# Kernel tuning notes

Measured on AMD Instinct MI355X. Metric: run time of the kernel, lower is better.

## Reference

```python
import jax, jax.numpy as jnp
import numpy as np

N, F, U, R, B, M = 8192, 64, 64, 4, 20, 512


def setup_inputs() -> dict:
    key = jax.random.key(0)
    ks = jax.random.split(key, 6)
    features = jax.random.normal(ks[0], (1, N, F), dtype=jnp.float32)
    out_indices = jax.random.randint(ks[1], (1, M), 0, N, dtype=jnp.int64)
    # normalized adjacency per relation; scale keeps activations O(1)
    adjacency = jax.random.uniform(ks[2], (R, N, N), dtype=jnp.float32) / N
    bases = jax.random.normal(ks[3], (F, U, B), dtype=jnp.float32) * (1.0 / np.sqrt(F * B))
    coefficients = jax.random.normal(ks[4], (R, B), dtype=jnp.float32)
    self_kernel = jax.random.normal(ks[5], (F, U), dtype=jnp.float32) * (1.0 / np.sqrt(F))
    bias = jnp.zeros((U,), dtype=jnp.float32)
    return {
        "features": features,
        "out_indices": out_indices,
        "adjacency": adjacency,
        "bases": bases,
        "coefficients": coefficients,
        "self_kernel": self_kernel,
        "bias": bias,
    }


def reference(features, out_indices, adjacency, bases, coefficients, self_kernel, bias):
    # features: (1, N, F); adjacency: (R, N, N)
    x = features[0]  # (N, F) -- full-batch, batch dim is 1
    # basis decomposition: W_r = sum_k bases[:, :, k] * coeff[r, k]
    W = jnp.einsum("fuk,rk->rfu", bases, coefficients)  # (R, F, U)
    xw = jnp.einsum("nf,rfu->rnu", x, W)               # (R, N, U)
    agg = jnp.einsum("rnm,rmu->nu", adjacency, xw)      # sum_r A_r @ (X W_r)
    out = agg + x @ self_kernel + bias                   # (N, U)
    out = jax.nn.relu(out)
    # final_layer=False: return all node features with batch dim restored
    return out[None]  # (1, N, U)
```

## Files before the change

### kernel.cpp

```cpp
#include <hip/hip_runtime.h>


typedef float v4f __attribute__((ext_vector_type(4)));
typedef unsigned int v4u __attribute__((ext_vector_type(4)));
typedef short v8s __attribute__((ext_vector_type(8)));

__device__ __forceinline__ unsigned short f2bf(float f) {
  unsigned int u = __builtin_bit_cast(unsigned int, f);
  return (unsigned short)((u + 0x7fffu + ((u >> 16) & 1u)) >> 16);
}

__device__ __forceinline__ void gload16(const void* g, void* l) {
  __builtin_amdgcn_global_load_lds((const __attribute__((address_space(1))) void*)g,
                                   (__attribute__((address_space(3))) void*)l, 16, 0, 0);
}

__device__ __forceinline__ void gload16nt(const void* g, void* l) {
  __builtin_amdgcn_global_load_lds((const __attribute__((address_space(1))) void*)g,
                                   (__attribute__((address_space(3))) void*)l, 16, 0, 2);
}

__global__ __launch_bounds__(256) void rgcn_wk(const float* __restrict__ bases,
                                               const float* __restrict__ coef,
                                               float* __restrict__ W) {
  int i = blockIdx.x * 256 + threadIdx.x;
  int r = i >> 12;
  int fu = i & 4095;
  float s = 0.f;
#pragma unroll
  for (int k = 0; k < 20; ++k) s += bases[fu * 20 + k] * coef[r * 20 + k];
  W[i] = s;
}

__global__ __launch_bounds__(256) void rgcn_prep(const float* __restrict__ x,
                                                 const float* __restrict__ W,
                                                 const float* __restrict__ sk,
                                                 const float* __restrict__ bias,
                                                 unsigned short* __restrict__ xwf,
                                                 float* __restrict__ selfout) {
  __shared__ float lx[2048];
  __shared__ unsigned short lxw[8192];
  const int t = threadIdx.x;
  const int blk = blockIdx.x;
  const int n0 = blk * 32;
  for (int i = t; i < 2048; i += 256) lx[i] = x[(size_t)n0 * 64 + i];
  __syncthreads();
  const int u = t & 63, rq = t >> 6;
  float acc[8][5];
#pragma unroll
  for (int p = 0; p < 8; ++p)
#pragma unroll
    for (int c = 0; c < 5; ++c) acc[p][c] = 0.f;
  const float* wu = W + u;
  const float* sku = sk + u;
#pragma unroll 4
  for (int f = 0; f < 64; ++f) {
    float w0 = wu[f * 64];
    float w1 = wu[4096 + f * 64];
    float w2 = wu[8192 + f * 64];
    float w3 = wu[12288 + f * 64];
    float w4 = sku[f * 64];
#pragma unroll
    for (int p = 0; p < 8; ++p) {
      float xv = lx[(rq * 8 + p) * 64 + f];
      acc[p][0] += xv * w0;
      acc[p][1] += xv * w1;
      acc[p][2] += xv * w2;
      acc[p][3] += xv * w3;
      acc[p][4] += xv * w4;
    }
  }
  const float bu = bias[u];
#pragma unroll
  for (int p = 0; p < 8; ++p) {
    int km = rq * 8 + p;
    selfout[(size_t)(n0 + km) * 64 + u] = acc[p][4] + bu;
    int idx = (u >> 4) * 512 + ((km >> 3) * 16 + (u & 15)) * 8 + (km & 7);
#pragma unroll
    for (int r = 0; r < 4; ++r) lxw[r * 2048 + idx] = f2bf(acc[p][r]);
  }
  __syncthreads();
  const unsigned int* lsrc = (const unsigned int*)lxw;
  unsigned int* gdst = (unsigned int*)xwf;
  for (int i = t; i < 4096; i += 256) {
    int r = i >> 10, q = i & 1023;
    gdst[(size_t)(r * 256 + blk) * 1024 + q] = lsrc[i];
  }
}


#define PACK8(S, X0, X1)          \
  {                               \
    S[0] = (short)f2bf(X0.x);     \
    S[1] = (short)f2bf(X0.y);     \
    S[2] = (short)f2bf(X0.z);     \
    S[3] = (short)f2bf(X0.w);     \
    S[4] = (short)f2bf(X1.x);     \
    S[5] = (short)f2bf(X1.y);     \
    S[6] = (short)f2bf(X1.z);     \
    S[7] = (short)f2bf(X1.w);     \
  }

#define STAGE(P)                                          \
  {                                                       \
    char* ab = Wb + (P)*16384;                            \
    gload16nt(aps0, ab);                                  \
    gload16nt(aps1, ab + 1024);                           \
    gload16nt(aps2, ab + 2048);                           \
    gload16nt(aps3, ab + 3072);                           \
    gload16nt(aps4, ab + 4096);                           \
    gload16nt(aps5, ab + 5120);                           \
    gload16nt(aps6, ab + 6144);                           \
    gload16nt(aps7, ab + 7168);                           \
    char* bb = ab + 8192;                                 \
    gload16(bsrc, bb);                                    \
    gload16(bsrc + 512, bb + 1024);                       \
    gload16(bsrc + 1024, bb + 2048);                      \
    gload16(bsrc + 1536, bb + 3072);                      \
    gload16(bsrc + 2048, bb + 4096);                      \
    gload16(bsrc + 2560, bb + 5120);                      \
    gload16(bsrc + 3072, bb + 6144);                      \
    gload16(bsrc + 3584, bb + 7168);                      \
    aps0 += 64; aps1 += 64; aps2 += 64; aps3 += 64;       \
    aps4 += 64; aps5 += 64; aps6 += 64; aps7 += 64;       \
    bsrc += 4096;                                         \
  }

#define MFMA8(AF0, AF1, B0, B1, B2, B3)                                          \
  {                                                                              \
    acc00 = __builtin_amdgcn_mfma_f32_16x16x32_bf16(AF0, B0, acc00, 0, 0, 0);    \
    acc01 = __builtin_amdgcn_mfma_f32_16x16x32_bf16(AF0, B1, acc01, 0, 0, 0);    \
    acc02 = __builtin_amdgcn_mfma_f32_16x16x32_bf16(AF0, B2, acc02, 0, 0, 0);    \
    acc03 = __builtin_amdgcn_mfma_f32_16x16x32_bf16(AF0, B3, acc03, 0, 0, 0);    \
    acc10 = __builtin_amdgcn_mfma_f32_16x16x32_bf16(AF1, B0, acc10, 0, 0, 0);    \
    acc11 = __builtin_amdgcn_mfma_f32_16x16x32_bf16(AF1, B1, acc11, 0, 0, 0);    \
    acc12 = __builtin_amdgcn_mfma_f32_16x16x32_bf16(AF1, B2, acc12, 0, 0, 0);    \
    acc13 = __builtin_amdgcn_mfma_f32_16x16x32_bf16(AF1, B3, acc13, 0, 0, 0);    \
  }

#define STEP(P, VMN, DO_STAGE)                                             \
  {                                                                        \
    asm volatile("s_waitcnt vmcnt(" #VMN ")" ::: "memory");                \
    __builtin_amdgcn_sched_barrier(0);                                     \
    const char* ap = Wb + (P)*16384;                                       \
    const char* bp = ap + 8192;                                            \
    v4f a000 = *(const v4f*)(ap + ao000);                                  \
    v4f a001 = *(const v4f*)(ap + ao001);                                  \
    v4f a010 = *(const v4f*)(ap + ao010);                                  \
    v4f a011 = *(const v4f*)(ap + ao011);                                  \
    v4f a100 = *(const v4f*)(ap + ao100);                                  \
    v4f a101 = *(const v4f*)(ap + ao101);                                  \
    v4f a110 = *(const v4f*)(ap + ao110);                                  \
    v4f a111 = *(const v4f*)(ap + ao111);                                  \
    v4u b00 = *(const v4u*)(bp + bo);                                      \
    v4u b01 = *(const v4u*)(bp + bo + 1024);                               \
    v4u b02 = *(const v4u*)(bp + bo + 2048);                               \
    v4u b03 = *(const v4u*)(bp + bo + 3072);                               \
    v4u b10 = *(const v4u*)(bp + bo + 4096);                               \
    v4u b11 = *(const v4u*)(bp + bo + 5120);                               \
    v4u b12 = *(const v4u*)(bp + bo + 6144);                               \
    v4u b13 = *(const v4u*)(bp + bo + 7168);                               \
    asm volatile("s_waitcnt lgkmcnt(0)" ::: "memory");                     \
    __builtin_amdgcn_sched_barrier(0);                                     \
    if (DO_STAGE) STAGE(P)                                                 \
    v8s af0, af1;                                                          \
    PACK8(af0, a000, a001);                                                \
    PACK8(af1, a010, a011);                                                \
    MFMA8(af0, af1, __builtin_bit_cast(v8s, b00), __builtin_bit_cast(v8s, b01), \
          __builtin_bit_cast(v8s, b02), __builtin_bit_cast(v8s, b03));     \
    PACK8(af0, a100, a101);                                                \
    PACK8(af1, a110, a111);                                                \
    MFMA8(af0, af1, __builtin_bit_cast(v8s, b10), __builtin_bit_cast(v8s, b11), \
          __builtin_bit_cast(v8s, b12), __builtin_bit_cast(v8s, b13));     \
  }

#define STORE_FRAG(ACC, RF, UT)                                        \
  red[w][((RF)*16 + lhi * 4 + 0) * 64 + (UT)*16 + l15] = ACC.x;        \
  red[w][((RF)*16 + lhi * 4 + 1) * 64 + (UT)*16 + l15] = ACC.y;        \
  red[w][((RF)*16 + lhi * 4 + 2) * 64 + (UT)*16 + l15] = ACC.z;        \
  red[w][((RF)*16 + lhi * 4 + 3) * 64 + (UT)*16 + l15] = ACC.w;

__global__ __launch_bounds__(256, 1) void rgcn_main(const float* __restrict__ A,
                                                    const unsigned short* __restrict__ xwf,
                                                    float* __restrict__ out) {
  __shared__ __align__(16) char smem[131072];
  const int tid = threadIdx.x;
  const int n0 = blockIdx.x * 32;
  const int w = tid >> 6;
  const int l = tid & 63;
  const int l15 = l & 15, lhi = l >> 4;

  const float* aps0;
  const float* aps1;
  const float* aps2;
  const float* aps3;
  const float* aps4;
  const float* aps5;
  const float* aps6;
  const float* aps7;
  {
    const float* base = A + ((size_t)w * 8192 + (size_t)n0) * 8192;
#define APS_INIT(J, P)                                                        \
    {                                                                         \
      int rr = (J)*4 + lhi;                                                   \
      int c = l15 ^ (rr & 7);                                                 \
      P = base + (size_t)rr * 8192 + c * 4;                                   \
    }
    APS_INIT(0, aps0) APS_INIT(1, aps1) APS_INIT(2, aps2) APS_INIT(3, aps3)
    APS_INIT(4, aps4) APS_INIT(5, aps5) APS_INIT(6, aps6) APS_INIT(7, aps7)
#undef APS_INIT
  }
  const unsigned short* bsrc = xwf + (size_t)w * 524288 + (size_t)l * 8;

  char* Wb = smem + w * 32768;

#define AOFF(G, RF, H) ((((RF)*16 + l15) * 16 + (((G)*8 + 2 * lhi + (H)) ^ (l15 & 7))) * 16)
  const int ao000 = AOFF(0, 0, 0), ao001 = AOFF(0, 0, 1);
  const int ao010 = AOFF(0, 1, 0), ao011 = AOFF(0, 1, 1);
  const int ao100 = AOFF(1, 0, 0), ao101 = AOFF(1, 0, 1);
  const int ao110 = AOFF(1, 1, 0), ao111 = AOFF(1, 1, 1);
#undef AOFF
  const int bo = l * 16;

  v4f acc00 = {0.f, 0.f, 0.f, 0.f}, acc01 = {0.f, 0.f, 0.f, 0.f};
  v4f acc02 = {0.f, 0.f, 0.f, 0.f}, acc03 = {0.f, 0.f, 0.f, 0.f};
  v4f acc10 = {0.f, 0.f, 0.f, 0.f}, acc11 = {0.f, 0.f, 0.f, 0.f};
  v4f acc12 = {0.f, 0.f, 0.f, 0.f}, acc13 = {0.f, 0.f, 0.f, 0.f};

  STAGE(0)
  STAGE(1)
  for (int t = 0; t < 63; ++t) {
    STEP(0, 16, 1)
    STEP(1, 16, 1)
  }
  STEP(0, 16, 0)
  STEP(1, 0, 0)

  __syncthreads();
  float(*red)[2048] = (float(*)[2048])smem;
  STORE_FRAG(acc00, 0, 0)
  STORE_FRAG(acc01, 0, 1)
  STORE_FRAG(acc02, 0, 2)
  STORE_FRAG(acc03, 0, 3)
  STORE_FRAG(acc10, 1, 0)
  STORE_FRAG(acc11, 1, 1)
  STORE_FRAG(acc12, 1, 2)
  STORE_FRAG(acc13, 1, 3)
  __syncthreads();
#pragma unroll
  for (int p = 0; p < 8; ++p) {
    int i = tid + 256 * p;
    float v = red[0][i] + red[1][i] + red[2][i] + red[3][i] + out[(size_t)n0 * 64 + i];
    out[(size_t)n0 * 64 + i] = fmaxf(v, 0.f);
  }
}

extern "C" void kernel_launch(void* const* d_in, const int* in_sizes, int n_in,
                              void* d_out, int out_size, void* d_ws, size_t ws_size,
                              hipStream_t stream) {
  const float* feat = (const float*)d_in[0];
  const float* adj = (const float*)d_in[2];
  const float* bases = (const float*)d_in[3];
  const float* coef = (const float*)d_in[4];
  const float* sk = (const float*)d_in[5];
  const float* bias = (const float*)d_in[6];
  float* out = (float*)d_out;

  unsigned short* xwf = (unsigned short*)d_ws;
  float* W = (float*)((char*)d_ws + (4u << 20));

  rgcn_wk<<<64, 256, 0, stream>>>(bases, coef, W);
  rgcn_prep<<<256, 256, 0, stream>>>(feat, W, sk, bias, xwf, out);
  rgcn_main<<<256, 256, 0, stream>>>(adj, xwf, out);

  (void)in_sizes;
  (void)n_in;
  (void)out_size;
  (void)ws_size;
}
```

Baseline: 200.2 us.

## Load B fragments directly to registers and double the K-step per stage

The precomputed bf16 XW operand no longer goes through LDS. Each lane now loads its B fragments straight from global memory into registers, double-buffered and issued after the MFMAs. The freed LDS holds an A tile twice as wide (128 columns per stage), so each stage does twice the K work and the loop trip count halves. The goals are to remove the LDS round-trip for B and to amortise waits and barriers over more MFMAs. The cost is many more live VGPRs (32 v4u B registers plus 16 A pointers) and a vmcnt accounting that now mixes register and LDS loads, which risks spills or wrong wait counts.

New measurement: 195.0 us. 2.6% less time.

```diff
diff --git a/kernel.cpp b/kernel.cpp
--- a/kernel.cpp
+++ b/kernel.cpp
@@ -8,11 +8,6 @@
 __device__ __forceinline__ unsigned short f2bf(float f) {
   unsigned int u = __builtin_bit_cast(unsigned int, f);
   return (unsigned short)((u + 0x7fffu + ((u >> 16) & 1u)) >> 16);
-}
-
-__device__ __forceinline__ void gload16(const void* g, void* l) {
-  __builtin_amdgcn_global_load_lds((const __attribute__((address_space(1))) void*)g,
-                                   (__attribute__((address_space(3))) void*)l, 16, 0, 0);
 }
 
 __device__ __forceinline__ void gload16nt(const void* g, void* l) {
@@ -101,7 +96,7 @@
     S[7] = (short)f2bf(X1.w);     \
   }
 
-#define STAGE(P)                                          \
+#define STAGE_A(P)                                        \
   {                                                       \
     char* ab = Wb + (P)*16384;                            \
     gload16nt(aps0, ab);                                  \
@@ -112,18 +107,39 @@
     gload16nt(aps5, ab + 5120);                           \
     gload16nt(aps6, ab + 6144);                           \
     gload16nt(aps7, ab + 7168);                           \
-    char* bb = ab + 8192;                                 \
-    gload16(bsrc, bb);                                    \
-    gload16(bsrc + 512, bb + 1024);                       \
-    gload16(bsrc + 1024, bb + 2048);                      \
-    gload16(bsrc + 1536, bb + 3072);                      \
-    gload16(bsrc + 2048, bb + 4096);                      \
-    gload16(bsrc + 2560, bb + 5120);                      \
-    gload16(bsrc + 3072, bb + 6144);                      \
-    gload16(bsrc + 3584, bb + 7168);                      \
-    aps0 += 64; aps1 += 64; aps2 += 64; aps3 += 64;       \
-    aps4 += 64; aps5 += 64; aps6 += 64; aps7 += 64;       \
-    bsrc += 4096;                                         \
+    gload16nt(aps8, ab + 8192);                           \
+    gload16nt(aps9, ab + 9216);                           \
+    gload16nt(aps10, ab + 10240);                         \
+    gload16nt(aps11, ab + 11264);                         \
+    gload16nt(aps12, ab + 12288);                         \
+    gload16nt(aps13, ab + 13312);                         \
+    gload16nt(aps14, ab + 14336);                         \
+    gload16nt(aps15, ab + 15360);                         \
+    aps0 += 128; aps1 += 128; aps2 += 128; aps3 += 128;   \
+    aps4 += 128; aps5 += 128; aps6 += 128; aps7 += 128;   \
+    aps8 += 128; aps9 += 128; aps10 += 128; aps11 += 128; \
+    aps12 += 128; aps13 += 128; aps14 += 128; aps15 += 128; \
+  }
+
+#define BLOAD(P)                                    \
+  {                                                 \
+    b##P##_00 = *(const v4u*)(bsrc);                \
+    b##P##_01 = *(const v4u*)(bsrc + 512);          \
+    b##P##_02 = *(const v4u*)(bsrc + 1024);         \
+    b##P##_03 = *(const v4u*)(bsrc + 1536);         \
+    b##P##_10 = *(const v4u*)(bsrc + 2048);         \
+    b##P##_11 = *(const v4u*)(bsrc + 2560);         \
+    b##P##_12 = *(const v4u*)(bsrc + 3072);         \
+    b##P##_13 = *(const v4u*)(bsrc + 3584);         \
+    b##P##_20 = *(const v4u*)(bsrc + 4096);         \
+    b##P##_21 = *(const v4u*)(bsrc + 4608);         \
+    b##P##_22 = *(const v4u*)(bsrc + 5120);         \
+    b##P##_23 = *(const v4u*)(bsrc + 5632);         \
+    b##P##_30 = *(const v4u*)(bsrc + 6144);         \
+    b##P##_31 = *(const v4u*)(bsrc + 6656);         \
+    b##P##_32 = *(const v4u*)(bsrc + 7168);         \
+    b##P##_33 = *(const v4u*)(bsrc + 7680);         \
+    bsrc += 8192;                                   \
   }
 
 #define MFMA8(AF0, AF1, B0, B1, B2, B3)                                          \
@@ -138,12 +154,13 @@
     acc13 = __builtin_amdgcn_mfma_f32_16x16x32_bf16(AF1, B3, acc13, 0, 0, 0);    \
   }
 
+#define BC(X) __builtin_bit_cast(v8s, X)
+
 #define STEP(P, VMN, DO_STAGE)                                             \
   {                                                                        \
     asm volatile("s_waitcnt vmcnt(" #VMN ")" ::: "memory");                \
     __builtin_amdgcn_sched_barrier(0);                                     \
     const char* ap = Wb + (P)*16384;                                       \
-    const char* bp = ap + 8192;                                            \
     v4f a000 = *(const v4f*)(ap + ao000);                                  \
     v4f a001 = *(const v4f*)(ap + ao001);                                  \
     v4f a010 = *(const v4f*)(ap + ao010);                                  \
@@ -152,26 +169,31 @@
     v4f a101 = *(const v4f*)(ap + ao101);                                  \
     v4f a110 = *(const v4f*)(ap + ao110);                                  \
     v4f a111 = *(const v4f*)(ap + ao111);                                  \
-    v4u b00 = *(const v4u*)(bp + bo);                                      \
-    v4u b01 = *(const v4u*)(bp + bo + 1024);                               \
-    v4u b02 = *(const v4u*)(bp + bo + 2048);                               \
-    v4u b03 = *(const v4u*)(bp + bo + 3072);                               \
-    v4u b10 = *(const v4u*)(bp + bo + 4096);                               \
-    v4u b11 = *(const v4u*)(bp + bo + 5120);                               \
-    v4u b12 = *(const v4u*)(bp + bo + 6144);                               \
-    v4u b13 = *(const v4u*)(bp + bo + 7168);                               \
+    v4f a200 = *(const v4f*)(ap + ao200);                                  \
+    v4f a201 = *(const v4f*)(ap + ao201);                                  \
+    v4f a210 = *(const v4f*)(ap + ao210);                                  \
+    v4f a211 = *(const v4f*)(ap + ao211);                                  \
+    v4f a300 = *(const v4f*)(ap + ao300);                                  \
+    v4f a301 = *(const v4f*)(ap + ao301);                                  \
+    v4f a310 = *(const v4f*)(ap + ao310);                                  \
+    v4f a311 = *(const v4f*)(ap + ao311);                                  \
     asm volatile("s_waitcnt lgkmcnt(0)" ::: "memory");                     \
     __builtin_amdgcn_sched_barrier(0);                                     \
-    if (DO_STAGE) STAGE(P)                                                 \
+    if (DO_STAGE) STAGE_A(P)                                               \
     v8s af0, af1;                                                          \
     PACK8(af0, a000, a001);                                                \
     PACK8(af1, a010, a011);                                                \
-    MFMA8(af0, af1, __builtin_bit_cast(v8s, b00), __builtin_bit_cast(v8s, b01), \
-          __builtin_bit_cast(v8s, b02), __builtin_bit_cast(v8s, b03));     \
+    MFMA8(af0, af1, BC(b##P##_00), BC(b##P##_01), BC(b##P##_02), BC(b##P##_03)); \
     PACK8(af0, a100, a101);                                                \
     PACK8(af1, a110, a111);                                                \
-    MFMA8(af0, af1, __builtin_bit_cast(v8s, b10), __builtin_bit_cast(v8s, b11), \
-          __builtin_bit_cast(v8s, b12), __builtin_bit_cast(v8s, b13));     \
+    MFMA8(af0, af1, BC(b##P##_10), BC(b##P##_11), BC(b##P##_12), BC(b##P##_13)); \
+    PACK8(af0, a200, a201);                                                \
+    PACK8(af1, a210, a211);                                                \
+    MFMA8(af0, af1, BC(b##P##_20), BC(b##P##_21), BC(b##P##_22), BC(b##P##_23)); \
+    PACK8(af0, a300, a301);                                                \
+    PACK8(af1, a310, a311);                                                \
+    MFMA8(af0, af1, BC(b##P##_30), BC(b##P##_31), BC(b##P##_32), BC(b##P##_33)); \
+    if (DO_STAGE) BLOAD(P)                                                 \
   }
 
 #define STORE_FRAG(ACC, RF, UT)                                        \
@@ -190,50 +212,56 @@
   const int l = tid & 63;
   const int l15 = l & 15, lhi = l >> 4;
 
-  const float* aps0;
-  const float* aps1;
-  const float* aps2;
-  const float* aps3;
-  const float* aps4;
-  const float* aps5;
-  const float* aps6;
-  const float* aps7;
+  const float* aps0;  const float* aps1;  const float* aps2;  const float* aps3;
+  const float* aps4;  const float* aps5;  const float* aps6;  const float* aps7;
+  const float* aps8;  const float* aps9;  const float* aps10; const float* aps11;
+  const float* aps12; const float* aps13; const float* aps14; const float* aps15;
   {
     const float* base = A + ((size_t)w * 8192 + (size_t)n0) * 8192;
-#define APS_INIT(J, P)                                                        \
+#define APS_INIT(J, PTR)                                                      \
     {                                                                         \
-      int rr = (J)*4 + lhi;                                                   \
-      int c = l15 ^ (rr & 7);                                                 \
-      P = base + (size_t)rr * 8192 + c * 4;                                   \
+      int rr = (J)*2 + (l >> 5);                                              \
+      int c = (l & 31) ^ (rr & 7);                                            \
+      PTR = base + (size_t)rr * 8192 + c * 4;                                 \
     }
-    APS_INIT(0, aps0) APS_INIT(1, aps1) APS_INIT(2, aps2) APS_INIT(3, aps3)
-    APS_INIT(4, aps4) APS_INIT(5, aps5) APS_INIT(6, aps6) APS_INIT(7, aps7)
+    APS_INIT(0, aps0)   APS_INIT(1, aps1)   APS_INIT(2, aps2)   APS_INIT(3, aps3)
+    APS_INIT(4, aps4)   APS_INIT(5, aps5)   APS_INIT(6, aps6)   APS_INIT(7, aps7)
+    APS_INIT(8, aps8)   APS_INIT(9, aps9)   APS_INIT(10, aps10) APS_INIT(11, aps11)
+    APS_INIT(12, aps12) APS_INIT(13, aps13) APS_INIT(14, aps14) APS_INIT(15, aps15)
 #undef APS_INIT
   }
   const unsigned short* bsrc = xwf + (size_t)w * 524288 + (size_t)l * 8;
 
   char* Wb = smem + w * 32768;
 
-#define AOFF(G, RF, H) ((((RF)*16 + l15) * 16 + (((G)*8 + 2 * lhi + (H)) ^ (l15 & 7))) * 16)
+#define AOFF(G, RF, H) ((((RF)*16 + l15) * 32 + (((G)*8 + 2 * lhi + (H)) ^ (l15 & 7))) * 16)
   const int ao000 = AOFF(0, 0, 0), ao001 = AOFF(0, 0, 1);
   const int ao010 = AOFF(0, 1, 0), ao011 = AOFF(0, 1, 1);
   const int ao100 = AOFF(1, 0, 0), ao101 = AOFF(1, 0, 1);
   const int ao110 = AOFF(1, 1, 0), ao111 = AOFF(1, 1, 1);
+  const int ao200 = AOFF(2, 0, 0), ao201 = AOFF(2, 0, 1);
+  const int ao210 = AOFF(2, 1, 0), ao211 = AOFF(2, 1, 1);
+  const int ao300 = AOFF(3, 0, 0), ao301 = AOFF(3, 0, 1);
+  const int ao310 = AOFF(3, 1, 0), ao311 = AOFF(3, 1, 1);
 #undef AOFF
-  const int bo = l * 16;
+
+  v4u b0_00, b0_01, b0_02, b0_03, b0_10, b0_11, b0_12, b0_13;
+  v4u b0_20, b0_21, b0_22, b0_23, b0_30, b0_31, b0_32, b0_33;
+  v4u b1_00, b1_01, b1_02, b1_03, b1_10, b1_11, b1_12, b1_13;
+  v4u b1_20, b1_21, b1_22, b1_23, b1_30, b1_31, b1_32, b1_33;
 
   v4f acc00 = {0.f, 0.f, 0.f, 0.f}, acc01 = {0.f, 0.f, 0.f, 0.f};
   v4f acc02 = {0.f, 0.f, 0.f, 0.f}, acc03 = {0.f, 0.f, 0.f, 0.f};
   v4f acc10 = {0.f, 0.f, 0.f, 0.f}, acc11 = {0.f, 0.f, 0.f, 0.f};
   v4f acc12 = {0.f, 0.f, 0.f, 0.f}, acc13 = {0.f, 0.f, 0.f, 0.f};
 
-  STAGE(0)
-  STAGE(1)
-  for (int t = 0; t < 63; ++t) {
-    STEP(0, 16, 1)
-    STEP(1, 16, 1)
-  }
-  STEP(0, 16, 0)
+  STAGE_A(0) BLOAD(0)
+  STAGE_A(1) BLOAD(1)
+  for (int t = 0; t < 31; ++t) {
+    STEP(0, 32, 1)
+    STEP(1, 32, 1)
+  }
+  STEP(0, 32, 0)
   STEP(1, 0, 0)
 
   __syncthreads();
```
